# Performance work log

Measured on AMD Instinct MI355X. Metric: run time of the kernel, lower is better.

Reference implementation:

```python
import jax, jax.numpy as jnp
import numpy as np

B, T, F = 32, 128, 128      # batch, time, num_features
NF = 8                      # num_filters
KW = 5                      # kernel_width
NC = F * NF                 # num_cells = 1024
NCLS = 1000                 # num_classes
PAD = KW // 2
EPS = 1e-5


def setup_inputs() -> dict:
    key = jax.random.key(0)
    ks = jax.random.split(key, 12)
    rn = lambda k, shape, s=1.0: jax.random.normal(k, shape, dtype=jnp.float32) * s
    st = (B, NF, 1, NC)
    zc = lambda: jnp.zeros((NF,), jnp.float32)
    oc = lambda: jnp.ones((NF,), jnp.float32)
    inp = {
        "x": rn(ks[0], (B, T, F)),
        "s": rn(ks[1], st),                       # init=1.0 -> std 1 normal
        "n": jnp.zeros(st, jnp.float32),
        "d": jnp.zeros(st, jnp.float32),
        "h": jnp.zeros(st, jnp.float32),
        "a_max": jnp.full(st, -1e38, jnp.float32),  # torch fills a_max with -1e38
        "x_resize_w": rn(ks[2], (NC, F), 0.05),     # Linear(num_features->num_cells), no bias
        "g_w": rn(ks[3], (NF, NF + 1, 1, KW), 0.1), "g_b": zc(), "g_gamma": oc(), "g_beta": zc(),
        "u_w": rn(ks[4], (NF, 1, 1, KW), 0.1),      "u_b": zc(), "u_gamma": oc(), "u_beta": zc(),
        "a_w": rn(ks[5], (NF, NF + 1, 1, KW), 0.1), "a_b": zc(), "a_gamma": oc(), "a_beta": zc(),
        "dec_w": rn(ks[6], (NF, NF + 1, 1, KW), 0.1), "dec_b": zc(), "dec_gamma": oc(), "dec_beta": zc(),
        "o_w": rn(ks[7], (NCLS, NC * NF), 0.01),
        "o_b": jnp.zeros((NCLS,), jnp.float32),
    }
    return inp


def _conv(x, w, b):
    # x: [B, C_in, 1, NC]; w: [C_out, C_in, 1, KW]; 'same' padding on width (kw odd)
    y = jax.lax.conv_general_dilated(x, w, window_strides=(1, 1),
                                     padding=[(0, 0), (PAD, PAD)],
                                     dimension_numbers=("NCHW", "OIHW", "NCHW"))
    return y + b[None, :, None, None]


def _bn(x, gamma, beta):
    # BatchNorm2d in training mode: per-channel batch stats over (N, H, W), biased var
    mu = jnp.mean(x, axis=(0, 2, 3), keepdims=True)
    var = jnp.mean((x - mu) ** 2, axis=(0, 2, 3), keepdims=True)
    return gamma[None, :, None, None] * (x - mu) * jax.lax.rsqrt(var + EPS) + beta[None, :, None, None]


def reference(x, s, n, d, h, a_max,
              x_resize_w,
              g_w, g_b, g_gamma, g_beta,
              u_w, u_b, u_gamma, u_beta,
              a_w, a_b, a_gamma, a_beta,
              dec_w, dec_b, dec_gamma, dec_beta,
              o_w, o_b):
    h0 = h + jnp.tanh(s)

    def step(carry, x_t):
        h_t, n_t, d_t, am = carry
        xr = (x_t @ x_resize_w.T)[:, None, None, :]    # [B,1,1,NC]
        xh = jnp.concatenate([xr, h_t], axis=1)        # [B,NF+1,1,NC]
        g_t = _bn(_conv(xh, g_w, g_b), g_gamma, g_beta)
        u_t = _bn(_conv(xr, u_w, u_b), u_gamma, u_beta)
        a_t = _bn(_conv(xh, a_w, a_b), a_gamma, a_beta)
        dec = jax.nn.sigmoid(_bn(_conv(xh, dec_w, dec_b), dec_gamma, dec_beta))
        ed = jnp.exp(-dec)
        z_t = u_t * jnp.tanh(g_t)
        a_new = jnp.maximum(am * ed, a_t)              # torch: max(a_max*exp(-decay), a_t)
        exp_diff = jnp.exp(am - a_new)
        exp_scaled = jnp.exp(a_t - a_new)
        n_new = n_t * ed * exp_diff + z_t * exp_scaled
        d_new = d_t * ed * exp_diff + exp_scaled
        h_new = jnp.tanh(n_new / d_new)
        return (h_new, n_new, d_new, a_new), None

    (h_T, n_T, d_T, am_T), _ = jax.lax.scan(step, (h0, n, d, a_max), jnp.swapaxes(x, 0, 1))
    outs = h_T.reshape(h_T.shape[0], -1) @ o_w.T + o_b  # [B, NCLS]
    return (outs, s, n_T, d_T, h_T, am_T)
```

## Files before the change

kernel.cpp:

```cpp
#include <hip/hip_runtime.h>


#define NBLK 256
#define NTHR 512

constexpr int Bb = 32, Tt = 128, NCc = 1024;
constexpr int PROW = 1032;
constexpr float EPSf  = 1e-5f;
constexpr float INV_N = 1.0f / 32768.0f;

constexpr size_t XR_OFF  = 0;
constexpr size_t XR_SZ   = (size_t)Tt * Bb * PROW;
constexpr size_t WT_OFF  = XR_OFF + XR_SZ;
constexpr size_t WT_SZ   = 131072;
constexpr size_t WPK_OFF = WT_OFF + WT_SZ;
constexpr size_t WPK_SZ  = 1280;
constexpr size_t ACC_OFF = WPK_OFF + WPK_SZ;
constexpr size_t ACC_SZ  = 3 * 16 * 64 * 32;
constexpr size_t SL2_OFF = ACC_OFF + ACC_SZ;
constexpr size_t SL2_SZ  = 2 * 32 * 8 * 2 * 64;
constexpr size_t CNT_OFF = SL2_OFF + SL2_SZ;
constexpr size_t STT_OFF = CNT_OFF + 512;

constexpr int OUT_S  = 32000;
constexpr int OUT_N  = 294144;
constexpr int OUT_D  = 556288;
constexpr int OUT_H  = 818432;
constexpr int OUT_AM = 1080576;

__device__ __forceinline__ float fast_tanh(float x) {
  float e = __expf(2.0f * x);
  return 1.0f - 2.0f / (e + 1.0f);
}

__device__ __forceinline__ unsigned long long pack2(float a, float b) {
  return (unsigned long long)__float_as_uint(a) |
         ((unsigned long long)__float_as_uint(b) << 32);
}

__global__ void prep_kernel(const float* __restrict__ w, float* __restrict__ wT,
                            const float* __restrict__ gw, const float* __restrict__ aw,
                            const float* __restrict__ dw, const float* __restrict__ uw,
                            float* __restrict__ wpack, float* __restrict__ acc3,
                            unsigned* __restrict__ cnt) {
  const int g = blockIdx.x * 256 + threadIdx.x;
  if (g < 131072) {
    const int c = g >> 7, k = g & 127;
    wT[k * 1024 + c] = w[g];
  }
  if (g < 1280) {
    const int f = g / 160, r = g % 160, ci = r >> 4, k = r & 15;
    float v = 0.f;
    if (ci < 9) {
      if (k < 5)       v = gw[(f * 9 + ci) * 5 + k];
      else if (k < 10) v = aw[(f * 9 + ci) * 5 + (k - 5)];
      else if (k < 15) v = dw[(f * 9 + ci) * 5 + (k - 10)];
    } else {
      if (k < 5)       v = uw[f * 5 + k];
    }
    wpack[g] = v;
  }
  if (g < (int)ACC_SZ) acc3[g] = 0.f;
  if (g < 2048) cnt[g] = 0u;
}

__global__ void __launch_bounds__(256) xr_kernel(const float* __restrict__ x,
                                                 const float* __restrict__ wT,
                                                 float* __restrict__ XR) {
  const int tb0 = blockIdx.x * 16;
  const int c0  = threadIdx.x * 4;
  float4 acc[16];
#pragma unroll
  for (int j = 0; j < 16; ++j) acc[j] = make_float4(0.f, 0.f, 0.f, 0.f);
#pragma unroll 4
  for (int k = 0; k < 128; ++k) {
    const float4 wv = *(const float4*)(wT + (size_t)k * 1024 + c0);
#pragma unroll
    for (int j = 0; j < 16; ++j) {
      const int tb = tb0 + j;
      const float xs = x[(size_t)(tb & 31) * 16384 + (size_t)(tb >> 5) * 128 + k];
      acc[j].x = fmaf(xs, wv.x, acc[j].x);
      acc[j].y = fmaf(xs, wv.y, acc[j].y);
      acc[j].z = fmaf(xs, wv.z, acc[j].z);
      acc[j].w = fmaf(xs, wv.w, acc[j].w);
    }
  }
#pragma unroll
  for (int j = 0; j < 16; ++j) {
    float* row = XR + (size_t)(tb0 + j) * PROW;
    *(float4*)(row + 4 + c0) = acc[j];
    if (threadIdx.x == 0)   { row[0] = row[1] = row[2] = row[3] = 0.f; }
    if (threadIdx.x == 255) { row[1028] = row[1029] = row[1030] = row[1031] = 0.f; }
  }
}

__global__ void __launch_bounds__(NTHR) scan_kernel(
    const float* __restrict__ XR, const float* __restrict__ wpack,
    float* acc3, float* slots2, unsigned* cnt, unsigned long long* stt,
    const float* __restrict__ s_in, const float* __restrict__ n_in,
    const float* __restrict__ d_in, const float* __restrict__ h_in,
    const float* __restrict__ am_in,
    const float* __restrict__ ggm, const float* __restrict__ gbt,
    const float* __restrict__ ugm, const float* __restrict__ ubt,
    const float* __restrict__ agm, const float* __restrict__ abt,
    const float* __restrict__ dgm, const float* __restrict__ dbt,
    float* __restrict__ out)
{
  const int tid  = (int)threadIdx.x;
  const int w    = tid >> 6;
  const int lane = tid & 63;

  if ((int)blockIdx.x == NBLK) {
    if (w == 0) {
      for (int t = 0; t < Tt; ++t) {
        const int p3 = t % 3;
        const unsigned tgt = 16u * (unsigned)(t + 1);
        for (;;) {
          unsigned c = 0u;
          if (lane < 16)
            c = __hip_atomic_load(cnt + lane * 32, __ATOMIC_RELAXED, __HIP_MEMORY_SCOPE_AGENT);
          if (__all((lane < 16) ? (int)(c >= tgt) : 1)) break;
          __builtin_amdgcn_s_sleep(1);
        }
        float s = 0.f;
        const float* ap = acc3 + p3 * 32768 + lane * 32;
#pragma unroll
        for (int r = 0; r < 16; ++r)
          s += __hip_atomic_load(ap + r * 2048, __ATOMIC_RELAXED, __HIP_MEMORY_SCOPE_AGENT);
        const unsigned long long pv =
            ((unsigned long long)(unsigned)(t + 1) << 32) |
            (unsigned long long)__float_as_uint(s);
#pragma unroll
        for (int cp = 0; cp < 4; ++cp)
          __hip_atomic_store(stt + cp * 64 + lane, pv, __ATOMIC_RELAXED, __HIP_MEMORY_SCOPE_AGENT);
      }
    }
    return;
  }

  const int bb   = (int)blockIdx.x >> 3;
  const int cc   = (int)blockIdx.x & 7;
  const int fu   = __builtin_amdgcn_readfirstlane(w);
  const float* __restrict__ wpk = wpack + fu * 160;

  const int c0    = 2 * lane;
  const int gc0   = cc * 128 + c0;
  const int cellbase = bb * 8192 + w * 1024 + gc0;
  const int rep16 = (int)blockIdx.x >> 4;
  const int scp   = (int)blockIdx.x & 3;

  const float ggamma = ggm[fu], gbeta = gbt[fu];
  const float ugamma = ugm[fu], ubeta = ubt[fu];
  const float agamma = agm[fu], abeta = abt[fu];
  const float dgamma = dgm[fu], dbeta = dbt[fu];

  __shared__ float hl[8][136];

  float nst[2], dst[2], amst[2], hv[2];
  float hn = 0.f, hd = 0.f, ham = -1e38f;
  const int  hloc   = (lane < 2) ? (lane - 2) : (128 + (lane - 2));
  const bool hvalid = (lane < 4) && ((lane < 2) ? (cc > 0) : (cc < 7));
  {
    const float2 n2 = *(const float2*)(n_in  + cellbase);
    const float2 d2 = *(const float2*)(d_in  + cellbase);
    const float2 a2 = *(const float2*)(am_in + cellbase);
    const float2 h2 = *(const float2*)(h_in  + cellbase);
    const float2 s2 = *(const float2*)(s_in  + cellbase);
    nst[0] = n2.x; nst[1] = n2.y;
    dst[0] = d2.x; dst[1] = d2.y;
    amst[0] = a2.x; amst[1] = a2.y;
    hv[0] = h2.x + fast_tanh(s2.x);
    hv[1] = h2.y + fast_tanh(s2.y);
    *(float2*)&hl[w][c0 + 4] = make_float2(hv[0], hv[1]);

    float hh0 = 0.f;
    if (hvalid) {
      const int gcell = bb * 8192 + w * 1024 + cc * 128 + hloc;
      hn  = n_in[gcell]; hd = d_in[gcell]; ham = am_in[gcell];
      hh0 = h_in[gcell] + fast_tanh(s_in[gcell]);
    }
    if (lane < 4) hl[w][hloc + 4] = hh0;
    if (lane >= 4 && lane < 8) {
      const int pidx = (lane == 4) ? 0 : (lane == 5) ? 1 : (lane == 6) ? 134 : 135;
      hl[w][pidx] = 0.f;
    }
  }

  float2 xa, xb, xc;
  {
    const float2* xr2 = (const float2*)(XR + (size_t)bb * PROW + 2 + gc0);
    xa = xr2[0]; xb = xr2[1]; xc = xr2[2];
  }
  __syncthreads();

  for (int t = 0; t < Tt; ++t) {
    const int p2 = t & 1;
    const int p3 = t % 3;

    float2 nxa, nxb, nxc;
    {
      const int tn = (t + 1 < Tt) ? (t + 1) : t;
      const float2* xr2 = (const float2*)(XR + (size_t)(tn * Bb + bb) * PROW + 2 + gc0);
      nxa = xr2[0]; nxb = xr2[1]; nxc = xr2[2];
    }

    float accg[2] = {0.f, 0.f}, acca[2] = {0.f, 0.f};
    float accd[2] = {0.f, 0.f}, accu[2] = {0.f, 0.f};

#pragma unroll
    for (int r = 0; r < 8; ++r) {
      const float2 qa = *(const float2*)&hl[r][c0 + 2];
      const float2 qb = *(const float2*)&hl[r][c0 + 4];
      const float2 qc = *(const float2*)&hl[r][c0 + 6];
      const float w6[6] = {qa.x, qa.y, qb.x, qb.y, qc.x, qc.y};
      const float* wp = wpk + (r + 1) * 16;
#pragma unroll
      for (int kw = 0; kw < 5; ++kw) {
        const float wg = wp[kw], wa = wp[5 + kw], wd = wp[10 + kw];
#pragma unroll
        for (int j = 0; j < 2; ++j) {
          const float v = w6[j + kw];
          accg[j] = fmaf(v, wg, accg[j]);
          acca[j] = fmaf(v, wa, acca[j]);
          accd[j] = fmaf(v, wd, accd[j]);
        }
      }
    }
    {
      const float w6[6] = {xa.x, xa.y, xb.x, xb.y, xc.x, xc.y};
      const float* wp = wpk;
      const float* wu = wpk + 144;
#pragma unroll
      for (int kw = 0; kw < 5; ++kw) {
        const float wg = wp[kw], wa = wp[5 + kw], wd = wp[10 + kw], wv = wu[kw];
#pragma unroll
        for (int j = 0; j < 2; ++j) {
          const float v = w6[j + kw];
          accg[j] = fmaf(v, wg, accg[j]);
          acca[j] = fmaf(v, wa, acca[j]);
          accd[j] = fmaf(v, wd, accd[j]);
          accu[j] = fmaf(v, wv, accu[j]);
        }
      }
    }

    if (lane == 0 || lane == 63) {
      const int side = lane ? 1 : 0;
      unsigned long long* bs = (unsigned long long*)
          (slots2 + ((((size_t)p2 * 32 + bb) * 8 + cc) * 2 + side) * 64 + w * 8);
      __hip_atomic_store(bs + 0, pack2(accg[0], accg[1]), __ATOMIC_RELAXED, __HIP_MEMORY_SCOPE_AGENT);
      __hip_atomic_store(bs + 1, pack2(acca[0], acca[1]), __ATOMIC_RELAXED, __HIP_MEMORY_SCOPE_AGENT);
      __hip_atomic_store(bs + 2, pack2(accd[0], accd[1]), __ATOMIC_RELAXED, __HIP_MEMORY_SCOPE_AGENT);
      __hip_atomic_store(bs + 3, pack2(accu[0], accu[1]), __ATOMIC_RELAXED, __HIP_MEMORY_SCOPE_AGENT);
    }

    {
      float ps[8];
      ps[0] = accg[0] + accg[1]; ps[1] = fmaf(accg[0], accg[0], accg[1] * accg[1]);
      ps[2] = acca[0] + acca[1]; ps[3] = fmaf(acca[0], acca[0], acca[1] * acca[1]);
      ps[4] = accd[0] + accd[1]; ps[5] = fmaf(accd[0], accd[0], accd[1] * accd[1]);
      ps[6] = accu[0] + accu[1]; ps[7] = fmaf(accu[0], accu[0], accu[1] * accu[1]);
#pragma unroll
      for (int m = 1; m <= 4; m <<= 1)
#pragma unroll
        for (int k = 0; k < 8; ++k) ps[k] += __shfl_xor(ps[k], m);
      const int l3 = lane & 7;
      const float a0 = (l3 & 1) ? ps[1] : ps[0];
      const float a1 = (l3 & 1) ? ps[3] : ps[2];
      const float a2 = (l3 & 1) ? ps[5] : ps[4];
      const float a3 = (l3 & 1) ? ps[7] : ps[6];
      const float b0 = (l3 & 2) ? a1 : a0;
      const float b1 = (l3 & 2) ? a3 : a2;
      float v = (l3 & 4) ? b1 : b0;
#pragma unroll
      for (int m = 8; m <= 32; m <<= 1) v += __shfl_xor(v, m);
      if (lane < 8)
        __hip_atomic_fetch_add(acc3 + p3 * 32768 + rep16 * 2048 + (w * 8 + lane) * 32,
                               v, __ATOMIC_RELAXED, __HIP_MEMORY_SCOPE_AGENT);
    }

    asm volatile("s_waitcnt vmcnt(0)" ::: "memory");
    __syncthreads();
    if (tid == 0)
      __hip_atomic_fetch_add(cnt + ((unsigned)blockIdx.x >> 4) * 32, 1u,
                             __ATOMIC_RELAXED, __HIP_MEMORY_SCOPE_AGENT);

    float sv = 0.f;
    {
      const unsigned long long* sp = stt + scp * 64 + w * 8;
      const unsigned tagv = (unsigned)(t + 1);
      unsigned long long pv = 0ull;
      for (;;) {
        if (lane < 8)
          pv = __hip_atomic_load(sp + lane, __ATOMIC_RELAXED, __HIP_MEMORY_SCOPE_AGENT);
        if (__all((lane < 8) ? (int)((unsigned)(pv >> 32) == tagv) : 1)) break;
        __builtin_amdgcn_s_sleep(1);
      }
      sv = __uint_as_float((unsigned)pv);
    }

    float graw = 0.f, araw = 0.f, draw = 0.f, uraw = 0.f;
    if (hvalid) {
      const int ncc  = (lane < 2) ? (cc - 1) : (cc + 1);
      const int nsid = (lane < 2) ? 1 : 0;
      const float* nb =
          slots2 + ((((size_t)p2 * 32 + bb) * 8 + ncc) * 2 + nsid) * 64 + w * 8 + (lane & 1);
      graw = __hip_atomic_load(nb + 0, __ATOMIC_RELAXED, __HIP_MEMORY_SCOPE_AGENT);
      araw = __hip_atomic_load(nb + 2, __ATOMIC_RELAXED, __HIP_MEMORY_SCOPE_AGENT);
      draw = __hip_atomic_load(nb + 4, __ATOMIC_RELAXED, __HIP_MEMORY_SCOPE_AGENT);
      uraw = __hip_atomic_load(nb + 6, __ATOMIC_RELAXED, __HIP_MEMORY_SCOPE_AGENT);
    }
    if (tid >= 256 && tid < 260) {
      const int idx = ((int)blockIdx.x << 2) + (tid - 256);
      __hip_atomic_store(acc3 + ((t + 2) % 3) * 32768 + (idx >> 6) * 2048 + (idx & 63) * 32,
                         0.f, __ATOMIC_RELAXED, __HIP_MEMORY_SCOPE_AGENT);
    }

    float st[8];
#pragma unroll
    for (int k = 0; k < 8; ++k) st[k] = __shfl(sv, k);

    const float mg = st[0] * INV_N; const float vg = fmaf(-mg, mg, st[1] * INV_N);
    const float sg = ggamma * rsqrtf(vg + EPSf); const float og = fmaf(-mg, sg, gbeta);
    const float ma = st[2] * INV_N; const float va = fmaf(-ma, ma, st[3] * INV_N);
    const float sa = agamma * rsqrtf(va + EPSf); const float oa = fmaf(-ma, sa, abeta);
    const float md = st[4] * INV_N; const float vd = fmaf(-md, md, st[5] * INV_N);
    const float sd = dgamma * rsqrtf(vd + EPSf); const float od = fmaf(-md, sd, dbeta);
    const float mu = st[6] * INV_N; const float vu = fmaf(-mu, mu, st[7] * INV_N);
    const float su = ugamma * rsqrtf(vu + EPSf); const float ou = fmaf(-mu, su, ubeta);

#pragma unroll
    for (int j = 0; j < 2; ++j) {
      const float gb = fmaf(accg[j], sg, og);
      const float ab = fmaf(acca[j], sa, oa);
      const float db = fmaf(accd[j], sd, od);
      const float ub = fmaf(accu[j], su, ou);
      const float dec = 1.0f / (1.0f + __expf(-db));
      const float ed  = __expf(-dec);
      const float z   = ub * fast_tanh(gb);
      const float anew = fmaxf(amst[j] * ed, ab);
      const float e1 = __expf(amst[j] - anew);
      const float e2 = __expf(ab - anew);
      const float ede1 = ed * e1;
      nst[j]  = fmaf(nst[j], ede1, z * e2);
      dst[j]  = fmaf(dst[j], ede1, e2);
      amst[j] = anew;
      hv[j]   = fast_tanh(nst[j] / dst[j]);
    }
    *(float2*)&hl[w][c0 + 4] = make_float2(hv[0], hv[1]);

    if (lane < 4) {
      float hres = 0.f;
      if (hvalid) {
        const float gb = fmaf(graw, sg, og);
        const float ab = fmaf(araw, sa, oa);
        const float db = fmaf(draw, sd, od);
        const float ub = fmaf(uraw, su, ou);
        const float dec = 1.0f / (1.0f + __expf(-db));
        const float ed  = __expf(-dec);
        const float z   = ub * fast_tanh(gb);
        const float anew = fmaxf(ham * ed, ab);
        const float e1 = __expf(ham - anew);
        const float e2 = __expf(ab - anew);
        const float ede1 = ed * e1;
        hn  = fmaf(hn, ede1, z * e2);
        hd  = fmaf(hd, ede1, e2);
        ham = anew;
        hres = fast_tanh(hn / hd);
      }
      hl[w][hloc + 4] = hres;
    }
    __syncthreads();

    xa = nxa; xb = nxb; xc = nxc;
  }

  {
    const float2 s2 = *(const float2*)(s_in + cellbase);
    *(float2*)(out + OUT_S  + cellbase) = s2;
    *(float2*)(out + OUT_N  + cellbase) = make_float2(nst[0], nst[1]);
    *(float2*)(out + OUT_D  + cellbase) = make_float2(dst[0], dst[1]);
    *(float2*)(out + OUT_H  + cellbase) = make_float2(hv[0], hv[1]);
    *(float2*)(out + OUT_AM + cellbase) = make_float2(amst[0], amst[1]);
  }
}

__global__ void __launch_bounds__(256) out_kernel(const float* __restrict__ outH,
                                                  const float* __restrict__ ow,
                                                  const float* __restrict__ ob,
                                                  float* __restrict__ out) {
  const int o   = blockIdx.x;
  const int tid = (int)threadIdx.x;
  const int wv  = tid >> 6;
  const int lane = tid & 63;

  float4 wr[8];
  {
    const float4* wq = (const float4*)(ow + (size_t)o * 8192 + tid * 32);
#pragma unroll
    for (int k = 0; k < 8; ++k) wr[k] = wq[k];
  }
  float acc[32];
#pragma unroll
  for (int b = 0; b < 32; ++b) {
    const float4* hq = (const float4*)(outH + (size_t)b * 8192 + tid * 32);
    float s0 = 0.f, s1 = 0.f;
#pragma unroll
    for (int k = 0; k < 8; k += 2) {
      const float4 h0 = hq[k], h1 = hq[k + 1];
      s0 = fmaf(h0.x, wr[k].x, s0);     s0 = fmaf(h0.y, wr[k].y, s0);
      s0 = fmaf(h0.z, wr[k].z, s0);     s0 = fmaf(h0.w, wr[k].w, s0);
      s1 = fmaf(h1.x, wr[k+1].x, s1);   s1 = fmaf(h1.y, wr[k+1].y, s1);
      s1 = fmaf(h1.z, wr[k+1].z, s1);   s1 = fmaf(h1.w, wr[k+1].w, s1);
    }
    acc[b] = s0 + s1;
  }
#pragma unroll
  for (int m = 1; m <= 32; m <<= 1)
#pragma unroll
    for (int b = 0; b < 32; ++b) acc[b] += __shfl_xor(acc[b], m);

  __shared__ float red[4][32];
  if (lane < 32) red[wv][lane] = acc[lane];
  __syncthreads();
  if (tid < 32)
    out[tid * 1000 + o] = red[0][tid] + red[1][tid] + red[2][tid] + red[3][tid] + ob[o];
}

extern "C" void kernel_launch(void* const* d_in, const int* in_sizes, int n_in,
                              void* d_out, int out_size, void* d_ws, size_t ws_size,
                              hipStream_t stream) {
  (void)in_sizes; (void)n_in; (void)out_size; (void)ws_size;
  const float* x   = (const float*)d_in[0];
  const float* s   = (const float*)d_in[1];
  const float* n_  = (const float*)d_in[2];
  const float* dd  = (const float*)d_in[3];
  const float* h   = (const float*)d_in[4];
  const float* am  = (const float*)d_in[5];
  const float* xrw = (const float*)d_in[6];
  const float* gw  = (const float*)d_in[7];
  const float* ggm = (const float*)d_in[9];
  const float* gbt = (const float*)d_in[10];
  const float* uw  = (const float*)d_in[11];
  const float* ugm = (const float*)d_in[13];
  const float* ubt = (const float*)d_in[14];
  const float* aw  = (const float*)d_in[15];
  const float* agm = (const float*)d_in[17];
  const float* abt = (const float*)d_in[18];
  const float* dw  = (const float*)d_in[19];
  const float* dgm = (const float*)d_in[21];
  const float* dbt = (const float*)d_in[22];
  const float* ow  = (const float*)d_in[23];
  const float* ob  = (const float*)d_in[24];
  float* out = (float*)d_out;
  float* ws  = (float*)d_ws;

  float* XR     = ws + XR_OFF;
  float* wT     = ws + WT_OFF;
  float* wpack  = ws + WPK_OFF;
  float* acc3   = ws + ACC_OFF;
  float* slots2 = ws + SL2_OFF;
  unsigned* cnt = (unsigned*)(ws + CNT_OFF);
  unsigned long long* stt = (unsigned long long*)(ws + STT_OFF);

  prep_kernel<<<dim3(512), dim3(256), 0, stream>>>(xrw, wT, gw, aw, dw, uw, wpack, acc3, cnt);
  xr_kernel<<<dim3(256), dim3(256), 0, stream>>>(x, wT, XR);

  void* args[] = { &XR, &wpack, &acc3, &slots2, &cnt, &stt, &s, &n_, &dd, &h, &am,
                   &ggm, &gbt, &ugm, &ubt, &agm, &abt, &dgm, &dbt, &out };
  hipError_t err = hipLaunchCooperativeKernel((void*)scan_kernel, dim3(NBLK + 1), dim3(NTHR),
                                              args, 0, stream);
  if (err != hipSuccess) {
    scan_kernel<<<dim3(NBLK + 1), dim3(NTHR), 0, stream>>>(XR, wpack, acc3, slots2, cnt, stt,
                                                           s, n_, dd, h, am,
                                                           ggm, gbt, ugm, ubt, agm, abt,
                                                           dgm, dbt, out);
  }

  out_kernel<<<dim3(1000), dim3(256), 0, stream>>>(out + OUT_H, ow, ob, out);
}
```

Measured before the change: 1.297 ms.

## Fuse BN stat accumulation and arrival counting into packed 64-bit fixed-point atomics

Replaces the float atomic-add BN statistics plus a separate per-group arrival counter (which needed a block-wide __syncthreads before the counter increment) with one 64-bit atomic per lane. Each atomic carries a count in the top 16 bits and a biased fixed-point sum below. The aggregator wave polls the same words it sums, so waiting and reading happen in one pass. This removes a barrier and one atomic round trip per time step. In exchange the sums become fixed-point with 2^-20 resolution and a bounded range, and slot zeroing now resets the packed words.

```diff
diff --git a/kernel.cpp b/kernel.cpp
--- a/kernel.cpp
+++ b/kernel.cpp
@@ -4,7 +4,7 @@
 #define NBLK 256
 #define NTHR 512
 
-constexpr int Bb = 32, Tt = 128, NCc = 1024;
+constexpr int Bb = 32, Tt = 128;
 constexpr int PROW = 1032;
 constexpr float EPSf  = 1e-5f;
 constexpr float INV_N = 1.0f / 32768.0f;
@@ -16,11 +16,10 @@
 constexpr size_t WPK_OFF = WT_OFF + WT_SZ;
 constexpr size_t WPK_SZ  = 1280;
 constexpr size_t ACC_OFF = WPK_OFF + WPK_SZ;
-constexpr size_t ACC_SZ  = 3 * 16 * 64 * 32;
+constexpr size_t ACC_SZ  = 98304;
 constexpr size_t SL2_OFF = ACC_OFF + ACC_SZ;
 constexpr size_t SL2_SZ  = 2 * 32 * 8 * 2 * 64;
-constexpr size_t CNT_OFF = SL2_OFF + SL2_SZ;
-constexpr size_t STT_OFF = CNT_OFF + 512;
+constexpr size_t STT_OFF = SL2_OFF + SL2_SZ;
 
 constexpr int OUT_S  = 32000;
 constexpr int OUT_N  = 294144;
@@ -42,7 +41,7 @@
                             const float* __restrict__ gw, const float* __restrict__ aw,
                             const float* __restrict__ dw, const float* __restrict__ uw,
                             float* __restrict__ wpack, float* __restrict__ acc3,
-                            unsigned* __restrict__ cnt) {
+                            float* __restrict__ sttf) {
   const int g = blockIdx.x * 256 + threadIdx.x;
   if (g < 131072) {
     const int c = g >> 7, k = g & 127;
@@ -61,7 +60,7 @@
     wpack[g] = v;
   }
   if (g < (int)ACC_SZ) acc3[g] = 0.f;
-  if (g < 2048) cnt[g] = 0u;
+  if (g < 512) sttf[g] = 0.f;
 }
 
 __global__ void __launch_bounds__(256) xr_kernel(const float* __restrict__ x,
@@ -96,7 +95,7 @@
 
 __global__ void __launch_bounds__(NTHR) scan_kernel(
     const float* __restrict__ XR, const float* __restrict__ wpack,
-    float* acc3, float* slots2, unsigned* cnt, unsigned long long* stt,
+    unsigned long long* stats, float* slots2, unsigned long long* stt,
     const float* __restrict__ s_in, const float* __restrict__ n_in,
     const float* __restrict__ d_in, const float* __restrict__ h_in,
     const float* __restrict__ am_in,
@@ -114,19 +113,24 @@
     if (w == 0) {
       for (int t = 0; t < Tt; ++t) {
         const int p3 = t % 3;
-        const unsigned tgt = 16u * (unsigned)(t + 1);
+        const unsigned long long* lp = stats + (size_t)p3 * 16384 + lane * 16;
+        unsigned long long v[16];
         for (;;) {
-          unsigned c = 0u;
-          if (lane < 16)
-            c = __hip_atomic_load(cnt + lane * 32, __ATOMIC_RELAXED, __HIP_MEMORY_SCOPE_AGENT);
-          if (__all((lane < 16) ? (int)(c >= tgt) : 1)) break;
+#pragma unroll
+          for (int r = 0; r < 16; ++r)
+            v[r] = __hip_atomic_load(lp + r * 1024, __ATOMIC_RELAXED, __HIP_MEMORY_SCOPE_AGENT);
+          unsigned csum = 0;
+#pragma unroll
+          for (int r = 0; r < 16; ++r) csum += (unsigned)(v[r] >> 48);
+          if (csum == 256u) break;
           __builtin_amdgcn_s_sleep(1);
         }
-        float s = 0.f;
-        const float* ap = acc3 + p3 * 32768 + lane * 32;
+        long long total = 0;
 #pragma unroll
         for (int r = 0; r < 16; ++r)
-          s += __hip_atomic_load(ap + r * 2048, __ATOMIC_RELAXED, __HIP_MEMORY_SCOPE_AGENT);
+          total += (long long)(v[r] & 0x0000FFFFFFFFFFFFull);
+        total -= (256ll << 43);
+        const float s = (float)((double)total * 9.5367431640625e-7);
         const unsigned long long pv =
             ((unsigned long long)(unsigned)(t + 1) << 32) |
             (unsigned long long)__float_as_uint(s);
@@ -254,6 +258,7 @@
       __hip_atomic_store(bs + 3, pack2(accu[0], accu[1]), __ATOMIC_RELAXED, __HIP_MEMORY_SCOPE_AGENT);
     }
 
+    float rv;
     {
       float ps[8];
       ps[0] = accg[0] + accg[1]; ps[1] = fmaf(accg[0], accg[0], accg[1] * accg[1]);
@@ -274,16 +279,26 @@
       float v = (l3 & 4) ? b1 : b0;
 #pragma unroll
       for (int m = 8; m <= 32; m <<= 1) v += __shfl_xor(v, m);
-      if (lane < 8)
-        __hip_atomic_fetch_add(acc3 + p3 * 32768 + rep16 * 2048 + (w * 8 + lane) * 32,
-                               v, __ATOMIC_RELAXED, __HIP_MEMORY_SCOPE_AGENT);
+      rv = v;
     }
 
     asm volatile("s_waitcnt vmcnt(0)" ::: "memory");
-    __syncthreads();
-    if (tid == 0)
-      __hip_atomic_fetch_add(cnt + ((unsigned)blockIdx.x >> 4) * 32, 1u,
-                             __ATOMIC_RELAXED, __HIP_MEMORY_SCOPE_AGENT);
+
+    if (lane < 8) {
+      const long long fx = llrint((double)rv * 1048576.0);
+      const unsigned long long enc =
+          (1ull << 48) + (unsigned long long)(fx + (1ll << 43));
+      (void)__hip_atomic_fetch_add(
+          stats + (size_t)p3 * 16384 + (size_t)rep16 * 1024 + (w * 8 + lane) * 16,
+          enc, __ATOMIC_RELAXED, __HIP_MEMORY_SCOPE_AGENT);
+    }
+
+    if (tid >= 256 && tid < 260) {
+      const int idx = ((int)blockIdx.x << 2) + (tid - 256);
+      __hip_atomic_store(stats + (size_t)((t + 2) % 3) * 16384 +
+                             (size_t)(idx >> 6) * 1024 + (idx & 63) * 16,
+                         0ull, __ATOMIC_RELAXED, __HIP_MEMORY_SCOPE_AGENT);
+    }
 
     float sv = 0.f;
     {
@@ -309,11 +324,6 @@
       araw = __hip_atomic_load(nb + 2, __ATOMIC_RELAXED, __HIP_MEMORY_SCOPE_AGENT);
       draw = __hip_atomic_load(nb + 4, __ATOMIC_RELAXED, __HIP_MEMORY_SCOPE_AGENT);
       uraw = __hip_atomic_load(nb + 6, __ATOMIC_RELAXED, __HIP_MEMORY_SCOPE_AGENT);
-    }
-    if (tid >= 256 && tid < 260) {
-      const int idx = ((int)blockIdx.x << 2) + (tid - 256);
-      __hip_atomic_store(acc3 + ((t + 2) % 3) * 32768 + (idx >> 6) * 2048 + (idx & 63) * 32,
-                         0.f, __ATOMIC_RELAXED, __HIP_MEMORY_SCOPE_AGENT);
     }
 
     float st[8];
@@ -458,20 +468,20 @@
   float* XR     = ws + XR_OFF;
   float* wT     = ws + WT_OFF;
   float* wpack  = ws + WPK_OFF;
-  float* acc3   = ws + ACC_OFF;
+  unsigned long long* stats = (unsigned long long*)(ws + ACC_OFF);
   float* slots2 = ws + SL2_OFF;
-  unsigned* cnt = (unsigned*)(ws + CNT_OFF);
   unsigned long long* stt = (unsigned long long*)(ws + STT_OFF);
 
-  prep_kernel<<<dim3(512), dim3(256), 0, stream>>>(xrw, wT, gw, aw, dw, uw, wpack, acc3, cnt);
+  prep_kernel<<<dim3(512), dim3(256), 0, stream>>>(xrw, wT, gw, aw, dw, uw, wpack,
+                                                   ws + ACC_OFF, ws + STT_OFF);
   xr_kernel<<<dim3(256), dim3(256), 0, stream>>>(x, wT, XR);
 
-  void* args[] = { &XR, &wpack, &acc3, &slots2, &cnt, &stt, &s, &n_, &dd, &h, &am,
+  void* args[] = { &XR, &wpack, &stats, &slots2, &stt, &s, &n_, &dd, &h, &am,
                    &ggm, &gbt, &ugm, &ubt, &agm, &abt, &dgm, &dbt, &out };
   hipError_t err = hipLaunchCooperativeKernel((void*)scan_kernel, dim3(NBLK + 1), dim3(NTHR),
                                               args, 0, stream);
   if (err != hipSuccess) {
-    scan_kernel<<<dim3(NBLK + 1), dim3(NTHR), 0, stream>>>(XR, wpack, acc3, slots2, cnt, stt,
+    scan_kernel<<<dim3(NBLK + 1), dim3(NTHR), 0, stream>>>(XR, wpack, stats, slots2, stt,
                                                            s, n_, dd, h, am,
                                                            ggm, gbt, ugm, ubt, agm, abt,
                                                            dgm, dbt, out);
```

Result: slower. 1.428 ms (+10.1%).
